# Performance work log

Hardware: AMD Instinct MI355X
Metric: run time of the kernel (lower is better)

The kernel has to match this reference:

```python
import jax, jax.numpy as jnp
import numpy as np
import math

B, N, M = 128, 32, 64           # batch, num_agents, num_other
OBS, ACT = 128, 16              # obs_input_dim, num_actions
D_QK = 128                      # obs_output_dim (== obs_output_dim_other)
D_AV = 64                       # obs_act_output_dim (== other)
F_IN = OBS + ACT                # obs_act_input_dim = 144


def _xavier(key, shape):
    fan_in, fan_out = shape[0], shape[1]
    limit = math.sqrt(6.0 / (fan_in + fan_out))
    return jax.random.uniform(key, shape, jnp.float32, -limit, limit)


def setup_inputs() -> dict:
    key = jax.random.key(0)
    ks = jax.random.split(key, 13)
    return {
        "states": jax.random.normal(ks[0], (B, N, OBS), jnp.float32),
        "policies": jax.random.uniform(ks[1], (B, N, ACT), jnp.float32),
        "actions": jax.random.uniform(ks[2], (B, N, ACT), jnp.float32),
        "states_other": jax.random.normal(ks[3], (B, M, OBS), jnp.float32),
        "actions_other": jax.random.uniform(ks[4], (B, M, ACT), jnp.float32),
        # weights stored as [in, out] (x @ W == nn.Linear without bias)
        "W_key": _xavier(ks[5], (OBS, D_QK)),
        "W_query": _xavier(ks[6], (OBS, D_QK)),
        "W_av": _xavier(ks[7], (F_IN, D_AV)),
        "W_key_other": _xavier(ks[8], (OBS, D_QK)),
        "W_query_other": _xavier(ks[9], (OBS, D_QK)),
        "W_av_other": _xavier(ks[10], (F_IN, D_AV)),
        "W_f1": _xavier(ks[11], (2 * D_AV, 64)),
        "W_f2": _xavier(ks[12], (64, 1)),
    }


def reference(states, policies, actions, states_other, actions_other,
              W_key, W_query, W_av, W_key_other, W_query_other,
              W_av_other, W_f1, W_f2):
    b, n, _ = states.shape
    obs_actions = jnp.concatenate([states, actions], axis=-1)   # [B,N,F_IN]
    obs_policy = jnp.concatenate([states, policies], axis=-1)   # [B,N,F_IN]

    key_obs = states @ W_key                                    # [B,N,D_QK]
    query_obs = states @ W_query                                # [B,N,D_QK]
    d_k = W_key.shape[1]
    weight = jax.nn.softmax(
        jnp.einsum('bid,bjd->bij', query_obs, key_obs) / math.sqrt(d_k), axis=-1)
    ret_weight = weight

    # place_policies is identity on (j,k): oap[b,j,k] = obs_policy[b,k] if j==k else obs_actions[b,k]
    eye = jnp.eye(n, dtype=states.dtype)[None, :, :, None]       # [1,N,N,1]
    oap = eye * obs_policy[:, None, :, :] + (1.0 - eye) * obs_actions[:, None, :, :]
    attention_values = jnp.tanh(oap @ W_av)                      # [B,N,N,D_AV] (j,k)

    # repeat-mul-sum == weighted reduction over k: wav[b,i,j,d] = sum_k w[b,i,k] av[b,j,k,d]
    wav = jnp.einsum('bik,bjkd->bijd', weight, attention_values)  # [B,N,N,D_AV]

    obs_actions_other = jnp.concatenate([states_other, actions_other], axis=-1)
    keys_other = states_other @ W_key_other                      # [B,M,D_QK]
    query_agent = states @ W_query_other                         # [B,N,D_QK]
    av_other = jnp.tanh(obs_actions_other @ W_av_other)          # [B,M,D_AV]
    d_k_o = W_key_other.shape[1]
    weight_other = jax.nn.softmax(
        jnp.einsum('bid,bmd->bim', query_agent, keys_other) / math.sqrt(d_k_o), axis=-1)
    wav_other = jnp.einsum('bim,bmd->bid', weight_other, av_other)  # [B,N,D_AV]

    # broadcast the per-agent other-branch features across the j axis for the concat
    wav_other_b = jnp.broadcast_to(wav_other[:, :, None, :], wav.shape[:-1] + (wav_other.shape[-1],))
    node_features = jnp.concatenate([wav, wav_other_b], axis=-1)  # [B,N,N,2*D_AV]

    h = jax.nn.leaky_relu(node_features @ W_f1, negative_slope=0.01)
    value = h @ W_f2                                              # [B,N,N,1]
    return value, ret_weight, weight_other
```

## Files before the change

### kernel.cpp

```cpp
#include <hip/hip_runtime.h>
#include <math.h>


#define WS_WQK   0
#define WS_WQKO  16384
#define WS_AVA   32768
#define WS_DELTA 294912
#define WS_AVO   557056
#define WS_DPROJ 1081344

#define INV_SQRT_DK 0.08838834764831845f

__global__ __launch_bounds__(256) void k1_pre(
    const float* __restrict__ g_states, const float* __restrict__ g_pol,
    const float* __restrict__ g_act, const float* __restrict__ g_so,
    const float* __restrict__ g_ao,
    const float* __restrict__ Wq, const float* __restrict__ Wk,
    const float* __restrict__ Wqo, const float* __restrict__ Wko,
    const float* __restrict__ W_av, const float* __restrict__ W_avo,
    float* __restrict__ ws)
{
  __shared__ float pool[8192];
  const int t = threadIdx.x;
  int blk = blockIdx.x;

  if (blk < 32) {
    const float* A; const float* Bm; float* O;
    if (blk < 16) { A = Wq;  Bm = Wk;  O = ws + WS_WQK; }
    else          { A = Wqo; Bm = Wko; O = ws + WS_WQKO; blk -= 16; }
    const int tr = (blk >> 2) << 5;
    const int tc = (blk & 3) << 5;
    float* sA = pool;
    float* sB = pool + 4096;
    const float4* a4 = (const float4*)(A + tr * 128);
    const float4* b4 = (const float4*)(Bm + tc * 128);
    #pragma unroll
    for (int u = 0; u < 4; ++u) {
      int f = t + u * 256;
      int r = f >> 5, c0 = (f & 31) << 2;
      float4 va = a4[f];
      sA[r*128 + ((c0+0) ^ r)] = va.x;
      sA[r*128 + ((c0+1) ^ r)] = va.y;
      sA[r*128 + ((c0+2) ^ r)] = va.z;
      sA[r*128 + ((c0+3) ^ r)] = va.w;
      float4 vb = b4[f];
      sB[r*128 + ((c0+0) ^ r)] = vb.x;
      sB[r*128 + ((c0+1) ^ r)] = vb.y;
      sB[r*128 + ((c0+2) ^ r)] = vb.z;
      sB[r*128 + ((c0+3) ^ r)] = vb.w;
    }
    __syncthreads();
    const int e = t & 31;
    #pragma unroll
    for (int rr = 0; rr < 4; ++rr) {
      const int cl = (t >> 5) + (rr << 3);
      float acc = 0.f;
      #pragma unroll 8
      for (int d = 0; d < 128; ++d)
        acc += sA[cl*128 + (d ^ cl)] * sB[e*128 + (d ^ e)];
      O[(tr + cl)*128 + tc + e] = acc;
    }
    return;
  }
  blk -= 32;

  if (blk < 256) {
    const int b = blk >> 1, k0 = (blk & 1) << 4;
    float* s_st = pool;
    float* s_ac = pool + 2048;
    float* s_po = pool + 2304;
    const float4* gs4 = (const float4*)(g_states + b*4096 + k0*128);
    #pragma unroll
    for (int u = 0; u < 2; ++u) {
      int f = t + u * 256;
      int r = f >> 5, c0 = (f & 31) << 2;
      float4 v = gs4[f];
      s_st[r*128 + ((c0+0) ^ r)] = v.x;
      s_st[r*128 + ((c0+1) ^ r)] = v.y;
      s_st[r*128 + ((c0+2) ^ r)] = v.z;
      s_st[r*128 + ((c0+3) ^ r)] = v.w;
    }
    if (t < 64)                ((float4*)s_ac)[t]      = ((const float4*)(g_act + b*512 + k0*16))[t];
    else if (t < 128)          ((float4*)s_po)[t - 64] = ((const float4*)(g_pol + b*512 + k0*16))[t - 64];
    __syncthreads();
    const int kk = t >> 4;
    const int d0 = (t & 15) << 2;
    float accB[4] = {0,0,0,0};
    #pragma unroll 4
    for (int c = 0; c < 128; ++c) {
      float sv = s_st[kk*128 + (c ^ kk)];
      float4 wv = *(const float4*)(W_av + c*64 + d0);
      accB[0] += sv*wv.x; accB[1] += sv*wv.y; accB[2] += sv*wv.z; accB[3] += sv*wv.w;
    }
    float accA[4], accP[4];
    #pragma unroll
    for (int q = 0; q < 4; ++q) { accA[q] = accB[q]; accP[q] = accB[q]; }
    #pragma unroll
    for (int cc = 0; cc < 16; ++cc) {
      float sa = s_ac[kk*16 + cc];
      float sp = s_po[kk*16 + cc];
      float4 wv = *(const float4*)(W_av + (128 + cc)*64 + d0);
      accA[0] += sa*wv.x; accA[1] += sa*wv.y; accA[2] += sa*wv.z; accA[3] += sa*wv.w;
      accP[0] += sp*wv.x; accP[1] += sp*wv.y; accP[2] += sp*wv.z; accP[3] += sp*wv.w;
    }
    #pragma unroll
    for (int q = 0; q < 4; ++q) {
      float va = tanhf(accA[q]);
      ws[WS_AVA   + b*2048 + (k0+kk)*64 + d0 + q] = va;
      ws[WS_DELTA + b*2048 + (k0+kk)*64 + d0 + q] = tanhf(accP[q]) - va;
    }
    return;
  }
  blk -= 256;

  {
    const int b = blk >> 1, m0 = (blk & 1) << 5;
    float* s_so = pool;
    float* s_ao = pool + 4096;
    const float4* gt4 = (const float4*)(g_so + (b*64 + m0) * 128);
    #pragma unroll
    for (int u = 0; u < 4; ++u) {
      int f = t + u * 256;
      int r = f >> 5, c0 = (f & 31) << 2;
      float4 v = gt4[f];
      s_so[r*128 + ((c0+0) ^ r)] = v.x;
      s_so[r*128 + ((c0+1) ^ r)] = v.y;
      s_so[r*128 + ((c0+2) ^ r)] = v.z;
      s_so[r*128 + ((c0+3) ^ r)] = v.w;
    }
    if (t < 128) ((float4*)s_ao)[t] = ((const float4*)(g_ao + (b*64 + m0)*16))[t];
    __syncthreads();
    const int mm = t >> 3;
    const int d0 = (t & 7) << 3;
    float acc[8] = {0,0,0,0,0,0,0,0};
    #pragma unroll 4
    for (int c = 0; c < 128; ++c) {
      float sv = s_so[mm*128 + (c ^ mm)];
      float4 w0 = *(const float4*)(W_avo + c*64 + d0);
      float4 w1 = *(const float4*)(W_avo + c*64 + d0 + 4);
      acc[0] += sv*w0.x; acc[1] += sv*w0.y; acc[2] += sv*w0.z; acc[3] += sv*w0.w;
      acc[4] += sv*w1.x; acc[5] += sv*w1.y; acc[6] += sv*w1.z; acc[7] += sv*w1.w;
    }
    #pragma unroll
    for (int cc = 0; cc < 16; ++cc) {
      float sv = s_ao[mm*16 + cc];
      float4 w0 = *(const float4*)(W_avo + (128 + cc)*64 + d0);
      float4 w1 = *(const float4*)(W_avo + (128 + cc)*64 + d0 + 4);
      acc[0] += sv*w0.x; acc[1] += sv*w0.y; acc[2] += sv*w0.z; acc[3] += sv*w0.w;
      acc[4] += sv*w1.x; acc[5] += sv*w1.y; acc[6] += sv*w1.z; acc[7] += sv*w1.w;
    }
    #pragma unroll
    for (int q = 0; q < 8; ++q)
      ws[WS_AVO + b*4096 + (m0+mm)*64 + d0 + q] = tanhf(acc[q]);
  }
}

__global__ __launch_bounds__(256) void k2_scores(
    const float* __restrict__ g_states, const float* __restrict__ g_so,
    const float* __restrict__ W_f1, float* __restrict__ ws,
    float* __restrict__ out)
{
  __shared__ float pool[6664];
  const int t = threadIdx.x;
  int blk = blockIdx.x;

  if (blk < 512) {
    const int b = blk >> 2, i0 = (blk & 3) << 3;
    float* s_st = pool;
    float* s_P  = pool + 4096;
    float* s_wo = pool + 6144;

    const float4* gs4 = (const float4*)(g_states + b * 4096);
    #pragma unroll
    for (int u = 0; u < 4; ++u) {
      int f = t + u * 256;
      int r = f >> 5, c0 = (f & 31) << 2;
      float4 v = gs4[f];
      s_st[r*128 + ((c0+0) ^ r)] = v.x;
      s_st[r*128 + ((c0+1) ^ r)] = v.y;
      s_st[r*128 + ((c0+2) ^ r)] = v.z;
      s_st[r*128 + ((c0+3) ^ r)] = v.w;
    }
    __syncthreads();

    {
      const int r = t >> 5, e0 = (t & 31) << 2, row = i0 + r;
      const float* wqk  = ws + WS_WQK;
      const float* wqko = ws + WS_WQKO;
      float4 a1 = {0,0,0,0}, a2 = {0,0,0,0};
      #pragma unroll 4
      for (int c = 0; c < 128; ++c) {
        float sv = s_st[row*128 + (c ^ row)];
        float4 w1 = *(const float4*)(wqk  + c*128 + e0);
        float4 w2 = *(const float4*)(wqko + c*128 + e0);
        a1.x += sv*w1.x; a1.y += sv*w1.y; a1.z += sv*w1.z; a1.w += sv*w1.w;
        a2.x += sv*w2.x; a2.y += sv*w2.y; a2.z += sv*w2.z; a2.w += sv*w2.w;
      }
      *(float4*)(s_P + r*256 + e0)       = a1;
      *(float4*)(s_P + r*256 + 128 + e0) = a2;
    }
    __syncthreads();

    {
      const int r = t >> 5, j = t & 31;
      float acc = 0.f;
      #pragma unroll 8
      for (int e = 0; e < 128; ++e)
        acc += s_P[r*256 + e] * s_st[j*128 + (e ^ j)];
      acc *= INV_SQRT_DK;
      float mx = acc;
      for (int off = 16; off; off >>= 1) mx = fmaxf(mx, __shfl_xor(mx, off, 32));
      float ev = __expf(acc - mx);
      float sum = ev;
      for (int off = 16; off; off >>= 1) sum += __shfl_xor(sum, off, 32);
      out[131072 + b*1024 + (i0 + r)*32 + j] = ev / sum;
    }
    __syncthreads();

    for (int tt = 0; tt < 2; ++tt) {
      const float4* gt4 = (const float4*)(g_so + (b*64 + tt*32) * 128);
      #pragma unroll
      for (int u = 0; u < 4; ++u) {
        int f = t + u * 256;
        int r = f >> 5, c0 = (f & 31) << 2;
        float4 v = gt4[f];
        s_st[r*128 + ((c0+0) ^ r)] = v.x;
        s_st[r*128 + ((c0+1) ^ r)] = v.y;
        s_st[r*128 + ((c0+2) ^ r)] = v.z;
        s_st[r*128 + ((c0+3) ^ r)] = v.w;
      }
      __syncthreads();
      const int r = t >> 5, m = t & 31;
      float acc = 0.f;
      #pragma unroll 8
      for (int c = 0; c < 128; ++c)
        acc += s_P[r*256 + 128 + c] * s_st[m*128 + (c ^ m)];
      s_wo[r*65 + tt*32 + m] = acc * INV_SQRT_DK;
      __syncthreads();
    }

    #pragma unroll
    for (int p = 0; p < 2; ++p) {
      const int r = (t >> 6) + (p << 2), l = t & 63;
      float v = s_wo[r*65 + l];
      float mx = v;
      for (int off = 32; off; off >>= 1) mx = fmaxf(mx, __shfl_xor(mx, off, 64));
      float ev = __expf(v - mx);
      float sum = ev;
      for (int off = 32; off; off >>= 1) sum += __shfl_xor(sum, off, 64);
      out[262144 + b*2048 + (i0 + r)*64 + l] = ev / sum;
    }
    return;
  }

  {
    const int b = blk - 512;
    float* s_d = pool;
    #pragma unroll
    for (int u = 0; u < 2; ++u)
      ((float4*)s_d)[t + u*256] = ((const float4*)(ws + WS_DELTA + b*2048))[t + u*256];
    __syncthreads();
    const int h = t & 63, j0 = (t >> 6) << 3;
    float acc[8] = {0,0,0,0,0,0,0,0};
    #pragma unroll 4
    for (int d = 0; d < 64; ++d) {
      float w1v = W_f1[d*64 + h];
      #pragma unroll
      for (int q = 0; q < 8; ++q)
        acc[q] += s_d[(j0+q)*64 + d] * w1v;
    }
    #pragma unroll
    for (int q = 0; q < 8; ++q)
      ws[WS_DPROJ + b*2048 + (j0+q)*64 + h] = acc[q];
  }
}

__global__ __launch_bounds__(256) void k3_value(
    const float* __restrict__ W_f1, const float* __restrict__ W_f2,
    const float* __restrict__ ws, float* __restrict__ out)
{
  __shared__ float s_avA[2048];
  __shared__ float s_avO[4096];
  __shared__ float s_dproj[2080];
  __shared__ float s_w[264];
  __shared__ float s_wo[520];
  __shared__ float s_S[512];
  __shared__ float s_wavo[512];
  __shared__ float s_base[512];
  __shared__ float s_wf2[64];
  const int t = threadIdx.x;
  const int b = blockIdx.x >> 2, i0 = (blockIdx.x & 3) << 3;

  #pragma unroll
  for (int u = 0; u < 2; ++u)
    ((float4*)s_avA)[t + u*256] = ((const float4*)(ws + WS_AVA + b*2048))[t + u*256];
  #pragma unroll
  for (int u = 0; u < 4; ++u)
    ((float4*)s_avO)[t + u*256] = ((const float4*)(ws + WS_AVO + b*4096))[t + u*256];
  #pragma unroll
  for (int u = 0; u < 8; ++u) {
    int idx = t + u*256;
    s_dproj[(idx >> 6)*65 + (idx & 63)] = ws[WS_DPROJ + b*2048 + idx];
  }
  {
    int li = t >> 5, j = t & 31;
    s_w[li*33 + j] = out[131072 + b*1024 + (i0 + li)*32 + j];
  }
  #pragma unroll
  for (int u = 0; u < 2; ++u) {
    int idx = t + u*256;
    int li = idx >> 6, m = idx & 63;
    s_wo[li*65 + m] = out[262144 + b*2048 + (i0 + li)*64 + m];
  }
  if (t < 64) s_wf2[t] = W_f2[t];
  __syncthreads();

  {
    const int d = t & 63, g = (t >> 6) << 1;
    float a0 = 0.f, a1 = 0.f;
    #pragma unroll 4
    for (int k = 0; k < 32; ++k) {
      float av = s_avA[k*64 + d];
      a0 += s_w[g*33 + k] * av;
      a1 += s_w[(g+1)*33 + k] * av;
    }
    s_S[g*64 + d] = a0; s_S[(g+1)*64 + d] = a1;
    float b0 = 0.f, b1 = 0.f;
    #pragma unroll 4
    for (int m = 0; m < 64; ++m) {
      float av = s_avO[m*64 + d];
      b0 += s_wo[g*65 + m] * av;
      b1 += s_wo[(g+1)*65 + m] * av;
    }
    s_wavo[g*64 + d] = b0; s_wavo[(g+1)*64 + d] = b1;
  }
  __syncthreads();

  {
    const int h = t & 63, g = (t >> 6) << 1;
    float a0 = 0.f, a1 = 0.f;
    #pragma unroll 4
    for (int d = 0; d < 64; ++d) {
      float w1v = W_f1[d*64 + h];
      float w2v = W_f1[(64 + d)*64 + h];
      a0 += s_S[g*64 + d]*w1v + s_wavo[g*64 + d]*w2v;
      a1 += s_S[(g+1)*64 + d]*w1v + s_wavo[(g+1)*64 + d]*w2v;
    }
    s_base[g*64 + h] = a0; s_base[(g+1)*64 + h] = a1;
  }
  __syncthreads();

  {
    const int i = t >> 5, j = t & 31;
    const float wij = s_w[i*33 + j];
    float acc = 0.f;
    #pragma unroll 4
    for (int h = 0; h < 64; ++h) {
      float pre = s_base[i*64 + h] + wij * s_dproj[j*65 + h];
      float hv = pre > 0.f ? pre : 0.01f * pre;
      acc += hv * s_wf2[h];
    }
    out[b*1024 + (i0 + i)*32 + j] = acc;
  }
}

extern "C" void kernel_launch(void* const* d_in, const int* in_sizes, int n_in,
                              void* d_out, int out_size, void* d_ws, size_t ws_size,
                              hipStream_t stream) {
  const float* states        = (const float*)d_in[0];
  const float* policies      = (const float*)d_in[1];
  const float* actions       = (const float*)d_in[2];
  const float* states_other  = (const float*)d_in[3];
  const float* actions_other = (const float*)d_in[4];
  const float* W_key         = (const float*)d_in[5];
  const float* W_query       = (const float*)d_in[6];
  const float* W_av          = (const float*)d_in[7];
  const float* W_key_other   = (const float*)d_in[8];
  const float* W_query_other = (const float*)d_in[9];
  const float* W_av_other    = (const float*)d_in[10];
  const float* W_f1          = (const float*)d_in[11];
  const float* W_f2          = (const float*)d_in[12];
  float* out = (float*)d_out;
  float* ws  = (float*)d_ws;

  k1_pre<<<544, 256, 0, stream>>>(states, policies, actions, states_other,
                                  actions_other, W_query, W_key,
                                  W_query_other, W_key_other, W_av, W_av_other,
                                  ws);
  k2_scores<<<640, 256, 0, stream>>>(states, states_other, W_f1, ws, out);
  k3_value<<<512, 256, 0, stream>>>(W_f1, W_f2, ws, out);
}
```

Before: 137.9 us.

## Fuse score and value kernels, move delta projection into preprocessing kernel

After: 132.2 us. 1.04x faster.

```diff
diff --git a/kernel.cpp b/kernel.cpp
--- a/kernel.cpp
+++ b/kernel.cpp
@@ -1,15 +1,17 @@
 #include <hip/hip_runtime.h>
 #include <math.h>
-
 
 #define WS_WQK   0
 #define WS_WQKO  16384
 #define WS_AVA   32768
-#define WS_DELTA 294912
-#define WS_AVO   557056
-#define WS_DPROJ 1081344
+#define WS_AVO   294912
+#define WS_DPROJ 819200
 
 #define INV_SQRT_DK 0.08838834764831845f
+
+__device__ __forceinline__ float dot4(float4 a, float4 b) {
+  return a.x*b.x + a.y*b.y + a.z*b.z + a.w*b.w;
+}
 
 __global__ __launch_bounds__(256) void k1_pre(
     const float* __restrict__ g_states, const float* __restrict__ g_pol,
@@ -18,9 +20,9 @@
     const float* __restrict__ Wq, const float* __restrict__ Wk,
     const float* __restrict__ Wqo, const float* __restrict__ Wko,
     const float* __restrict__ W_av, const float* __restrict__ W_avo,
-    float* __restrict__ ws)
+    const float* __restrict__ W_f1, float* __restrict__ ws)
 {
-  __shared__ float pool[8192];
+  __shared__ float pool[8448];
   const int t = threadIdx.x;
   int blk = blockIdx.x;
 
@@ -31,115 +33,151 @@
     const int tr = (blk >> 2) << 5;
     const int tc = (blk & 3) << 5;
     float* sA = pool;
-    float* sB = pool + 4096;
+    float* sB = pool + 4224;
     const float4* a4 = (const float4*)(A + tr * 128);
     const float4* b4 = (const float4*)(Bm + tc * 128);
     #pragma unroll
     for (int u = 0; u < 4; ++u) {
       int f = t + u * 256;
-      int r = f >> 5, c0 = (f & 31) << 2;
-      float4 va = a4[f];
-      sA[r*128 + ((c0+0) ^ r)] = va.x;
-      sA[r*128 + ((c0+1) ^ r)] = va.y;
-      sA[r*128 + ((c0+2) ^ r)] = va.z;
-      sA[r*128 + ((c0+3) ^ r)] = va.w;
-      float4 vb = b4[f];
-      sB[r*128 + ((c0+0) ^ r)] = vb.x;
-      sB[r*128 + ((c0+1) ^ r)] = vb.y;
-      sB[r*128 + ((c0+2) ^ r)] = vb.z;
-      sB[r*128 + ((c0+3) ^ r)] = vb.w;
-    }
-    __syncthreads();
-    const int e = t & 31;
-    #pragma unroll
-    for (int rr = 0; rr < 4; ++rr) {
-      const int cl = (t >> 5) + (rr << 3);
-      float acc = 0.f;
-      #pragma unroll 8
-      for (int d = 0; d < 128; ++d)
-        acc += sA[cl*128 + (d ^ cl)] * sB[e*128 + (d ^ e)];
-      O[(tr + cl)*128 + tc + e] = acc;
-    }
+      int r = f >> 5, c4 = f & 31;
+      *(float4*)(sA + r*132 + c4*4) = a4[f];
+      *(float4*)(sB + r*132 + c4*4) = b4[f];
+    }
+    __syncthreads();
+    const int e = t & 31, cl0 = t >> 5;
+    float acc[4] = {0,0,0,0};
+    #pragma unroll 4
+    for (int d4 = 0; d4 < 32; ++d4) {
+      float4 bv = *(const float4*)(sB + e*132 + d4*4);
+      #pragma unroll
+      for (int rr = 0; rr < 4; ++rr) {
+        float4 av = *(const float4*)(sA + (cl0 + rr*8)*132 + d4*4);
+        acc[rr] += dot4(av, bv);
+      }
+    }
+    #pragma unroll
+    for (int rr = 0; rr < 4; ++rr)
+      O[(tr + cl0 + rr*8)*128 + tc + e] = acc[rr];
     return;
   }
   blk -= 32;
 
-  if (blk < 256) {
-    const int b = blk >> 1, k0 = (blk & 1) << 4;
+  if (blk < 128) {
+    const int b = blk;
     float* s_st = pool;
-    float* s_ac = pool + 2048;
-    float* s_po = pool + 2304;
-    const float4* gs4 = (const float4*)(g_states + b*4096 + k0*128);
-    #pragma unroll
-    for (int u = 0; u < 2; ++u) {
+    float* s_ac = pool + 4224;
+    float* s_po = pool + 4736;
+    float* s_dl = pool + 5248;
+    const float4* gs4 = (const float4*)(g_states + b*4096);
+    #pragma unroll
+    for (int u = 0; u < 4; ++u) {
       int f = t + u * 256;
-      int r = f >> 5, c0 = (f & 31) << 2;
-      float4 v = gs4[f];
-      s_st[r*128 + ((c0+0) ^ r)] = v.x;
-      s_st[r*128 + ((c0+1) ^ r)] = v.y;
-      s_st[r*128 + ((c0+2) ^ r)] = v.z;
-      s_st[r*128 + ((c0+3) ^ r)] = v.w;
-    }
-    if (t < 64)                ((float4*)s_ac)[t]      = ((const float4*)(g_act + b*512 + k0*16))[t];
-    else if (t < 128)          ((float4*)s_po)[t - 64] = ((const float4*)(g_pol + b*512 + k0*16))[t - 64];
-    __syncthreads();
-    const int kk = t >> 4;
-    const int d0 = (t & 15) << 2;
-    float accB[4] = {0,0,0,0};
-    #pragma unroll 4
-    for (int c = 0; c < 128; ++c) {
-      float sv = s_st[kk*128 + (c ^ kk)];
-      float4 wv = *(const float4*)(W_av + c*64 + d0);
-      accB[0] += sv*wv.x; accB[1] += sv*wv.y; accB[2] += sv*wv.z; accB[3] += sv*wv.w;
-    }
-    float accA[4], accP[4];
-    #pragma unroll
-    for (int q = 0; q < 4; ++q) { accA[q] = accB[q]; accP[q] = accB[q]; }
-    #pragma unroll
-    for (int cc = 0; cc < 16; ++cc) {
-      float sa = s_ac[kk*16 + cc];
-      float sp = s_po[kk*16 + cc];
-      float4 wv = *(const float4*)(W_av + (128 + cc)*64 + d0);
-      accA[0] += sa*wv.x; accA[1] += sa*wv.y; accA[2] += sa*wv.z; accA[3] += sa*wv.w;
-      accP[0] += sp*wv.x; accP[1] += sp*wv.y; accP[2] += sp*wv.z; accP[3] += sp*wv.w;
-    }
-    #pragma unroll
-    for (int q = 0; q < 4; ++q) {
-      float va = tanhf(accA[q]);
-      ws[WS_AVA   + b*2048 + (k0+kk)*64 + d0 + q] = va;
-      ws[WS_DELTA + b*2048 + (k0+kk)*64 + d0 + q] = tanhf(accP[q]) - va;
+      int r = f >> 5, c4 = f & 31;
+      *(float4*)(s_st + r*132 + c4*4) = gs4[f];
+    }
+    if (t < 128)      ((float4*)s_ac)[t]       = ((const float4*)(g_act + b*512))[t];
+    else              ((float4*)s_po)[t - 128] = ((const float4*)(g_pol + b*512))[t - 128];
+    __syncthreads();
+    {
+      const int kk = t >> 3;
+      const int d0 = (t & 7) << 3;
+      float accB[8] = {0,0,0,0,0,0,0,0};
+      #pragma unroll 2
+      for (int c4 = 0; c4 < 32; ++c4) {
+        float4 s4 = *(const float4*)(s_st + kk*132 + c4*4);
+        const float sv[4] = {s4.x, s4.y, s4.z, s4.w};
+        #pragma unroll
+        for (int k = 0; k < 4; ++k) {
+          int c = c4*4 + k;
+          float4 w0 = *(const float4*)(W_av + c*64 + d0);
+          float4 w1 = *(const float4*)(W_av + c*64 + d0 + 4);
+          accB[0] += sv[k]*w0.x; accB[1] += sv[k]*w0.y;
+          accB[2] += sv[k]*w0.z; accB[3] += sv[k]*w0.w;
+          accB[4] += sv[k]*w1.x; accB[5] += sv[k]*w1.y;
+          accB[6] += sv[k]*w1.z; accB[7] += sv[k]*w1.w;
+        }
+      }
+      float accA[8], accP[8];
+      #pragma unroll
+      for (int q = 0; q < 8; ++q) { accA[q] = accB[q]; accP[q] = accB[q]; }
+      #pragma unroll
+      for (int cc = 0; cc < 16; ++cc) {
+        float sa = s_ac[kk*16 + cc];
+        float sp = s_po[kk*16 + cc];
+        float4 w0 = *(const float4*)(W_av + (128 + cc)*64 + d0);
+        float4 w1 = *(const float4*)(W_av + (128 + cc)*64 + d0 + 4);
+        accA[0] += sa*w0.x; accA[1] += sa*w0.y; accA[2] += sa*w0.z; accA[3] += sa*w0.w;
+        accA[4] += sa*w1.x; accA[5] += sa*w1.y; accA[6] += sa*w1.z; accA[7] += sa*w1.w;
+        accP[0] += sp*w0.x; accP[1] += sp*w0.y; accP[2] += sp*w0.z; accP[3] += sp*w0.w;
+        accP[4] += sp*w1.x; accP[5] += sp*w1.y; accP[6] += sp*w1.z; accP[7] += sp*w1.w;
+      }
+      float4 va0, va1, dl0, dl1;
+      va0.x = tanhf(accA[0]); va0.y = tanhf(accA[1]);
+      va0.z = tanhf(accA[2]); va0.w = tanhf(accA[3]);
+      va1.x = tanhf(accA[4]); va1.y = tanhf(accA[5]);
+      va1.z = tanhf(accA[6]); va1.w = tanhf(accA[7]);
+      dl0.x = tanhf(accP[0]) - va0.x; dl0.y = tanhf(accP[1]) - va0.y;
+      dl0.z = tanhf(accP[2]) - va0.z; dl0.w = tanhf(accP[3]) - va0.w;
+      dl1.x = tanhf(accP[4]) - va1.x; dl1.y = tanhf(accP[5]) - va1.y;
+      dl1.z = tanhf(accP[6]) - va1.z; dl1.w = tanhf(accP[7]) - va1.w;
+      *(float4*)(ws + WS_AVA + b*2048 + kk*64 + d0)     = va0;
+      *(float4*)(ws + WS_AVA + b*2048 + kk*64 + d0 + 4) = va1;
+      *(float4*)(s_dl + kk*68 + d0)     = dl0;
+      *(float4*)(s_dl + kk*68 + d0 + 4) = dl1;
+    }
+    __syncthreads();
+    {
+      const int h = t & 63;
+      const int j0 = (t >> 6) << 3;
+      float acc[8] = {0,0,0,0,0,0,0,0};
+      #pragma unroll 4
+      for (int d4 = 0; d4 < 16; ++d4) {
+        float w0 = W_f1[(d4*4+0)*64 + h];
+        float w1 = W_f1[(d4*4+1)*64 + h];
+        float w2 = W_f1[(d4*4+2)*64 + h];
+        float w3 = W_f1[(d4*4+3)*64 + h];
+        #pragma unroll
+        for (int q = 0; q < 8; ++q) {
+          float4 dv = *(const float4*)(s_dl + (j0+q)*68 + d4*4);
+          acc[q] += dv.x*w0 + dv.y*w1 + dv.z*w2 + dv.w*w3;
+        }
+      }
+      #pragma unroll
+      for (int q = 0; q < 8; ++q)
+        ws[WS_DPROJ + b*2048 + (j0+q)*64 + h] = acc[q];
     }
     return;
   }
-  blk -= 256;
+  blk -= 128;
 
   {
     const int b = blk >> 1, m0 = (blk & 1) << 5;
     float* s_so = pool;
-    float* s_ao = pool + 4096;
+    float* s_ao = pool + 4224;
     const float4* gt4 = (const float4*)(g_so + (b*64 + m0) * 128);
     #pragma unroll
     for (int u = 0; u < 4; ++u) {
       int f = t + u * 256;
-      int r = f >> 5, c0 = (f & 31) << 2;
-      float4 v = gt4[f];
-      s_so[r*128 + ((c0+0) ^ r)] = v.x;
-      s_so[r*128 + ((c0+1) ^ r)] = v.y;
-      s_so[r*128 + ((c0+2) ^ r)] = v.z;
-      s_so[r*128 + ((c0+3) ^ r)] = v.w;
+      int r = f >> 5, c4 = f & 31;
+      *(float4*)(s_so + r*132 + c4*4) = gt4[f];
     }
     if (t < 128) ((float4*)s_ao)[t] = ((const float4*)(g_ao + (b*64 + m0)*16))[t];
     __syncthreads();
     const int mm = t >> 3;
     const int d0 = (t & 7) << 3;
     float acc[8] = {0,0,0,0,0,0,0,0};
-    #pragma unroll 4
-    for (int c = 0; c < 128; ++c) {
-      float sv = s_so[mm*128 + (c ^ mm)];
-      float4 w0 = *(const float4*)(W_avo + c*64 + d0);
-      float4 w1 = *(const float4*)(W_avo + c*64 + d0 + 4);
-      acc[0] += sv*w0.x; acc[1] += sv*w0.y; acc[2] += sv*w0.z; acc[3] += sv*w0.w;
-      acc[4] += sv*w1.x; acc[5] += sv*w1.y; acc[6] += sv*w1.z; acc[7] += sv*w1.w;
+    #pragma unroll 2
+    for (int c4 = 0; c4 < 32; ++c4) {
+      float4 s4 = *(const float4*)(s_so + mm*132 + c4*4);
+      const float sv[4] = {s4.x, s4.y, s4.z, s4.w};
+      #pragma unroll
+      for (int k = 0; k < 4; ++k) {
+        int c = c4*4 + k;
+        float4 w0 = *(const float4*)(W_avo + c*64 + d0);
+        float4 w1 = *(const float4*)(W_avo + c*64 + d0 + 4);
+        acc[0] += sv[k]*w0.x; acc[1] += sv[k]*w0.y; acc[2] += sv[k]*w0.z; acc[3] += sv[k]*w0.w;
+        acc[4] += sv[k]*w1.x; acc[5] += sv[k]*w1.y; acc[6] += sv[k]*w1.z; acc[7] += sv[k]*w1.w;
+      }
     }
     #pragma unroll
     for (int cc = 0; cc < 16; ++cc) {
@@ -149,190 +187,168 @@
       acc[0] += sv*w0.x; acc[1] += sv*w0.y; acc[2] += sv*w0.z; acc[3] += sv*w0.w;
       acc[4] += sv*w1.x; acc[5] += sv*w1.y; acc[6] += sv*w1.z; acc[7] += sv*w1.w;
     }
-    #pragma unroll
-    for (int q = 0; q < 8; ++q)
-      ws[WS_AVO + b*4096 + (m0+mm)*64 + d0 + q] = tanhf(acc[q]);
+    float4 o0, o1;
+    o0.x = tanhf(acc[0]); o0.y = tanhf(acc[1]); o0.z = tanhf(acc[2]); o0.w = tanhf(acc[3]);
+    o1.x = tanhf(acc[4]); o1.y = tanhf(acc[5]); o1.z = tanhf(acc[6]); o1.w = tanhf(acc[7]);
+    *(float4*)(ws + WS_AVO + b*4096 + (m0+mm)*64 + d0)     = o0;
+    *(float4*)(ws + WS_AVO + b*4096 + (m0+mm)*64 + d0 + 4) = o1;
   }
 }
 
-__global__ __launch_bounds__(256) void k2_scores(
+__global__ __launch_bounds__(256) void k2_main(
     const float* __restrict__ g_states, const float* __restrict__ g_so,
-    const float* __restrict__ W_f1, float* __restrict__ ws,
-    float* __restrict__ out)
-{
-  __shared__ float pool[6664];
-  const int t = threadIdx.x;
-  int blk = blockIdx.x;
-
-  if (blk < 512) {
-    const int b = blk >> 2, i0 = (blk & 3) << 3;
-    float* s_st = pool;
-    float* s_P  = pool + 4096;
-    float* s_wo = pool + 6144;
-
-    const float4* gs4 = (const float4*)(g_states + b * 4096);
-    #pragma unroll
-    for (int u = 0; u < 4; ++u) {
-      int f = t + u * 256;
-      int r = f >> 5, c0 = (f & 31) << 2;
-      float4 v = gs4[f];
-      s_st[r*128 + ((c0+0) ^ r)] = v.x;
-      s_st[r*128 + ((c0+1) ^ r)] = v.y;
-      s_st[r*128 + ((c0+2) ^ r)] = v.z;
-      s_st[r*128 + ((c0+3) ^ r)] = v.w;
-    }
-    __syncthreads();
-
-    {
-      const int r = t >> 5, e0 = (t & 31) << 2, row = i0 + r;
-      const float* wqk  = ws + WS_WQK;
-      const float* wqko = ws + WS_WQKO;
-      float4 a1 = {0,0,0,0}, a2 = {0,0,0,0};
-      #pragma unroll 4
-      for (int c = 0; c < 128; ++c) {
-        float sv = s_st[row*128 + (c ^ row)];
-        float4 w1 = *(const float4*)(wqk  + c*128 + e0);
-        float4 w2 = *(const float4*)(wqko + c*128 + e0);
-        a1.x += sv*w1.x; a1.y += sv*w1.y; a1.z += sv*w1.z; a1.w += sv*w1.w;
-        a2.x += sv*w2.x; a2.y += sv*w2.y; a2.z += sv*w2.z; a2.w += sv*w2.w;
-      }
-      *(float4*)(s_P + r*256 + e0)       = a1;
-      *(float4*)(s_P + r*256 + 128 + e0) = a2;
-    }
-    __syncthreads();
-
-    {
-      const int r = t >> 5, j = t & 31;
-      float acc = 0.f;
-      #pragma unroll 8
-      for (int e = 0; e < 128; ++e)
-        acc += s_P[r*256 + e] * s_st[j*128 + (e ^ j)];
-      acc *= INV_SQRT_DK;
-      float mx = acc;
-      for (int off = 16; off; off >>= 1) mx = fmaxf(mx, __shfl_xor(mx, off, 32));
-      float ev = __expf(acc - mx);
-      float sum = ev;
-      for (int off = 16; off; off >>= 1) sum += __shfl_xor(sum, off, 32);
-      out[131072 + b*1024 + (i0 + r)*32 + j] = ev / sum;
-    }
-    __syncthreads();
-
-    for (int tt = 0; tt < 2; ++tt) {
-      const float4* gt4 = (const float4*)(g_so + (b*64 + tt*32) * 128);
-      #pragma unroll
-      for (int u = 0; u < 4; ++u) {
-        int f = t + u * 256;
-        int r = f >> 5, c0 = (f & 31) << 2;
-        float4 v = gt4[f];
-        s_st[r*128 + ((c0+0) ^ r)] = v.x;
-        s_st[r*128 + ((c0+1) ^ r)] = v.y;
-        s_st[r*128 + ((c0+2) ^ r)] = v.z;
-        s_st[r*128 + ((c0+3) ^ r)] = v.w;
-      }
-      __syncthreads();
-      const int r = t >> 5, m = t & 31;
-      float acc = 0.f;
-      #pragma unroll 8
-      for (int c = 0; c < 128; ++c)
-        acc += s_P[r*256 + 128 + c] * s_st[m*128 + (c ^ m)];
-      s_wo[r*65 + tt*32 + m] = acc * INV_SQRT_DK;
-      __syncthreads();
-    }
-
-    #pragma unroll
-    for (int p = 0; p < 2; ++p) {
-      const int r = (t >> 6) + (p << 2), l = t & 63;
-      float v = s_wo[r*65 + l];
-      float mx = v;
-      for (int off = 32; off; off >>= 1) mx = fmaxf(mx, __shfl_xor(mx, off, 64));
-      float ev = __expf(v - mx);
-      float sum = ev;
-      for (int off = 32; off; off >>= 1) sum += __shfl_xor(sum, off, 64);
-      out[262144 + b*2048 + (i0 + r)*64 + l] = ev / sum;
-    }
-    return;
-  }
-
-  {
-    const int b = blk - 512;
-    float* s_d = pool;
-    #pragma unroll
-    for (int u = 0; u < 2; ++u)
-      ((float4*)s_d)[t + u*256] = ((const float4*)(ws + WS_DELTA + b*2048))[t + u*256];
-    __syncthreads();
-    const int h = t & 63, j0 = (t >> 6) << 3;
-    float acc[8] = {0,0,0,0,0,0,0,0};
-    #pragma unroll 4
-    for (int d = 0; d < 64; ++d) {
-      float w1v = W_f1[d*64 + h];
-      #pragma unroll
-      for (int q = 0; q < 8; ++q)
-        acc[q] += s_d[(j0+q)*64 + d] * w1v;
-    }
-    #pragma unroll
-    for (int q = 0; q < 8; ++q)
-      ws[WS_DPROJ + b*2048 + (j0+q)*64 + h] = acc[q];
-  }
-}
-
-__global__ __launch_bounds__(256) void k3_value(
     const float* __restrict__ W_f1, const float* __restrict__ W_f2,
     const float* __restrict__ ws, float* __restrict__ out)
 {
-  __shared__ float s_avA[2048];
-  __shared__ float s_avO[4096];
-  __shared__ float s_dproj[2080];
-  __shared__ float s_w[264];
-  __shared__ float s_wo[520];
-  __shared__ float s_S[512];
-  __shared__ float s_wavo[512];
-  __shared__ float s_base[512];
-  __shared__ float s_wf2[64];
+  __shared__ float pool[11232];
+  float* s_st   = pool;
+  float* s_P1   = pool + 4352;
+  float* s_P2   = pool + 4352 + 1056;
+  float* s_avO  = pool;
+  float* s_avA  = pool + 4352;
+  float* s_dp   = pool + 6528;
+  float* s_w    = pool + 8704;
+  float* s_wo   = pool + 8992;
+  float* s_S    = pool + 9536;
+  float* s_wavo = pool + 10080;
+  float* s_base = pool + 10624;
+  float* s_wf2  = pool + 11168;
+
   const int t = threadIdx.x;
-  const int b = blockIdx.x >> 2, i0 = (blockIdx.x & 3) << 3;
-
-  #pragma unroll
-  for (int u = 0; u < 2; ++u)
-    ((float4*)s_avA)[t + u*256] = ((const float4*)(ws + WS_AVA + b*2048))[t + u*256];
-  #pragma unroll
-  for (int u = 0; u < 4; ++u)
-    ((float4*)s_avO)[t + u*256] = ((const float4*)(ws + WS_AVO + b*4096))[t + u*256];
-  #pragma unroll
-  for (int u = 0; u < 8; ++u) {
-    int idx = t + u*256;
-    s_dproj[(idx >> 6)*65 + (idx & 63)] = ws[WS_DPROJ + b*2048 + idx];
-  }
-  {
-    int li = t >> 5, j = t & 31;
-    s_w[li*33 + j] = out[131072 + b*1024 + (i0 + li)*32 + j];
-  }
+  const int b = blockIdx.x >> 2;
+  const int i0 = (blockIdx.x & 3) << 3;
+
   #pragma unroll
   for (int u = 0; u < 2; ++u) {
-    int idx = t + u*256;
-    int li = idx >> 6, m = idx & 63;
-    s_wo[li*65 + m] = out[262144 + b*2048 + (i0 + li)*64 + m];
-  }
-  if (t < 64) s_wf2[t] = W_f2[t];
-  __syncthreads();
-
-  {
-    const int d = t & 63, g = (t >> 6) << 1;
-    float a0 = 0.f, a1 = 0.f;
+    int f = t + u * 256;
+    int j = f >> 4, dq = f & 15;
+    *(float4*)(s_dp + j*68 + dq*4) = ((const float4*)(ws + WS_DPROJ + b*2048))[f];
+  }
+  if (t < 16) *(float4*)(s_wf2 + t*4) = ((const float4*)W_f2)[t];
+  {
+    const float4* gs4 = (const float4*)(g_states + b * 4096);
+    #pragma unroll
+    for (int u = 0; u < 4; ++u) {
+      int f = t + u * 256;
+      int r = f >> 5, c4 = f & 31;
+      *(float4*)(s_st + r*132 + c4*4) = gs4[f];
+    }
+  }
+  __syncthreads();
+
+  {
+    const int r = t >> 5, e0 = (t & 31) << 2, row = i0 + r;
+    const float* wqk  = ws + WS_WQK;
+    const float* wqko = ws + WS_WQKO;
+    float4 a1 = {0,0,0,0}, a2 = {0,0,0,0};
+    #pragma unroll 2
+    for (int c4 = 0; c4 < 32; ++c4) {
+      float4 s4 = *(const float4*)(s_st + row*132 + c4*4);
+      const float sv[4] = {s4.x, s4.y, s4.z, s4.w};
+      #pragma unroll
+      for (int k = 0; k < 4; ++k) {
+        int c = c4*4 + k;
+        float4 w1 = *(const float4*)(wqk  + c*128 + e0);
+        float4 w2 = *(const float4*)(wqko + c*128 + e0);
+        a1.x += sv[k]*w1.x; a1.y += sv[k]*w1.y; a1.z += sv[k]*w1.z; a1.w += sv[k]*w1.w;
+        a2.x += sv[k]*w2.x; a2.y += sv[k]*w2.y; a2.z += sv[k]*w2.z; a2.w += sv[k]*w2.w;
+      }
+    }
+    *(float4*)(s_P1 + r*132 + e0) = a1;
+    *(float4*)(s_P2 + r*132 + e0) = a2;
+  }
+  __syncthreads();
+
+  {
+    const int r = t >> 5, j = t & 31;
+    float acc = 0.f;
+    #pragma unroll 8
+    for (int e4 = 0; e4 < 32; ++e4) {
+      float4 p4  = *(const float4*)(s_P1 + r*132 + e4*4);
+      float4 st4 = *(const float4*)(s_st + j*132 + e4*4);
+      acc += dot4(p4, st4);
+    }
+    acc *= INV_SQRT_DK;
+    float mx = acc;
+    for (int off = 16; off; off >>= 1) mx = fmaxf(mx, __shfl_xor(mx, off, 32));
+    float ev = __expf(acc - mx);
+    float sum = ev;
+    for (int off = 16; off; off >>= 1) sum += __shfl_xor(sum, off, 32);
+    float wn = ev / sum;
+    out[131072 + b*1024 + (i0 + r)*32 + j] = wn;
+    s_w[r*36 + j] = wn;
+  }
+  __syncthreads();
+
+  for (int tt = 0; tt < 2; ++tt) {
+    const float4* gt4 = (const float4*)(g_so + (b*64 + tt*32) * 128);
+    #pragma unroll
+    for (int u = 0; u < 4; ++u) {
+      int f = t + u * 256;
+      int r = f >> 5, c4 = f & 31;
+      *(float4*)(s_st + r*132 + c4*4) = gt4[f];
+    }
+    __syncthreads();
+    const int r = t >> 5, m = t & 31;
+    float acc = 0.f;
+    #pragma unroll 8
+    for (int c4 = 0; c4 < 32; ++c4) {
+      float4 p4  = *(const float4*)(s_P2 + r*132 + c4*4);
+      float4 st4 = *(const float4*)(s_st + m*132 + c4*4);
+      acc += dot4(p4, st4);
+    }
+    s_wo[r*68 + tt*32 + m] = acc * INV_SQRT_DK;
+    __syncthreads();
+  }
+
+  #pragma unroll
+  for (int p = 0; p < 2; ++p) {
+    const int r = (t >> 6) + (p << 2), l = t & 63;
+    float v = s_wo[r*68 + l];
+    float mx = v;
+    for (int off = 32; off; off >>= 1) mx = fmaxf(mx, __shfl_xor(mx, off, 64));
+    float ev = __expf(v - mx);
+    float sum = ev;
+    for (int off = 32; off; off >>= 1) sum += __shfl_xor(sum, off, 64);
+    float wn = ev / sum;
+    out[262144 + b*2048 + (i0 + r)*64 + l] = wn;
+    s_wo[r*68 + l] = wn;
+  }
+  #pragma unroll
+  for (int u = 0; u < 2; ++u) {
+    int f = t + u * 256;
+    int k = f >> 4, dq = f & 15;
+    *(float4*)(s_avA + k*68 + dq*4) = ((const float4*)(ws + WS_AVA + b*2048))[f];
+  }
+  #pragma unroll
+  for (int u = 0; u < 4; ++u) {
+    int f = t + u * 256;
+    int m = f >> 4, dq = f & 15;
+    *(float4*)(s_avO + m*68 + dq*4) = ((const float4*)(ws + WS_AVO + b*4096))[f];
+  }
+  __syncthreads();
+
+  if (t < 128) {
+    const int i = t >> 4, dq = (t & 15) << 2;
+    float4 acc = {0,0,0,0};
     #pragma unroll 4
     for (int k = 0; k < 32; ++k) {
-      float av = s_avA[k*64 + d];
-      a0 += s_w[g*33 + k] * av;
-      a1 += s_w[(g+1)*33 + k] * av;
-    }
-    s_S[g*64 + d] = a0; s_S[(g+1)*64 + d] = a1;
-    float b0 = 0.f, b1 = 0.f;
+      float4 a4 = *(const float4*)(s_avA + k*68 + dq);
+      float wv = s_w[i*36 + k];
+      acc.x += wv*a4.x; acc.y += wv*a4.y; acc.z += wv*a4.z; acc.w += wv*a4.w;
+    }
+    *(float4*)(s_S + i*68 + dq) = acc;
+  } else {
+    const int tt2 = t - 128;
+    const int i = tt2 >> 4, dq = (tt2 & 15) << 2;
+    float4 acc = {0,0,0,0};
     #pragma unroll 4
     for (int m = 0; m < 64; ++m) {
-      float av = s_avO[m*64 + d];
-      b0 += s_wo[g*65 + m] * av;
-      b1 += s_wo[(g+1)*65 + m] * av;
-    }
-    s_wavo[g*64 + d] = b0; s_wavo[(g+1)*64 + d] = b1;
+      float4 a4 = *(const float4*)(s_avO + m*68 + dq);
+      float wv = s_wo[i*68 + m];
+      acc.x += wv*a4.x; acc.y += wv*a4.y; acc.z += wv*a4.z; acc.w += wv*a4.w;
+    }
+    *(float4*)(s_wavo + i*68 + dq) = acc;
   }
   __syncthreads();
 
@@ -343,22 +359,28 @@
     for (int d = 0; d < 64; ++d) {
       float w1v = W_f1[d*64 + h];
       float w2v = W_f1[(64 + d)*64 + h];
-      a0 += s_S[g*64 + d]*w1v + s_wavo[g*64 + d]*w2v;
-      a1 += s_S[(g+1)*64 + d]*w1v + s_wavo[(g+1)*64 + d]*w2v;
-    }
-    s_base[g*64 + h] = a0; s_base[(g+1)*64 + h] = a1;
+      a0 += s_S[g*68 + d]*w1v + s_wavo[g*68 + d]*w2v;
+      a1 += s_S[(g+1)*68 + d]*w1v + s_wavo[(g+1)*68 + d]*w2v;
+    }
+    s_base[g*68 + h] = a0;
+    s_base[(g+1)*68 + h] = a1;
   }
   __syncthreads();
 
   {
     const int i = t >> 5, j = t & 31;
-    const float wij = s_w[i*33 + j];
+    const float wij = s_w[i*36 + j];
     float acc = 0.f;
     #pragma unroll 4
-    for (int h = 0; h < 64; ++h) {
-      float pre = s_base[i*64 + h] + wij * s_dproj[j*65 + h];
-      float hv = pre > 0.f ? pre : 0.01f * pre;
-      acc += hv * s_wf2[h];
+    for (int hq = 0; hq < 16; ++hq) {
+      float4 b4 = *(const float4*)(s_base + i*68 + hq*4);
+      float4 d4 = *(const float4*)(s_dp + j*68 + hq*4);
+      float4 f4 = *(const float4*)(s_wf2 + hq*4);
+      float p0 = b4.x + wij*d4.x; p0 = p0 > 0.f ? p0 : 0.01f*p0;
+      float p1 = b4.y + wij*d4.y; p1 = p1 > 0.f ? p1 : 0.01f*p1;
+      float p2 = b4.z + wij*d4.z; p2 = p2 > 0.f ? p2 : 0.01f*p2;
+      float p3 = b4.w + wij*d4.w; p3 = p3 > 0.f ? p3 : 0.01f*p3;
+      acc += p0*f4.x + p1*f4.y + p2*f4.z + p3*f4.w;
     }
     out[b*1024 + (i0 + i)*32 + j] = acc;
   }
@@ -383,10 +405,9 @@
   float* out = (float*)d_out;
   float* ws  = (float*)d_ws;
 
-  k1_pre<<<544, 256, 0, stream>>>(states, policies, actions, states_other,
+  k1_pre<<<416, 256, 0, stream>>>(states, policies, actions, states_other,
                                   actions_other, W_query, W_key,
                                   W_query_other, W_key_other, W_av, W_av_other,
-                                  ws);
-  k2_scores<<<640, 256, 0, stream>>>(states, states_other, W_f1, ws, out);
-  k3_value<<<512, 256, 0, stream>>>(W_f1, W_f2, ws, out);
+                                  W_f1, ws);
+  k2_main<<<512, 256, 0, stream>>>(states, states_other, W_f1, W_f2, ws, out);
 }
```
